# Kernel optimization log

Measured on AMD Instinct MI355X. Metric: run time of the kernel, lower is better.

## Reference

```python
import jax, jax.numpy as jnp
import numpy as np

EMB = 512
HEAD = 64
B, S = 4, 4096


def setup_inputs() -> dict:
    key = jax.random.key(0)
    kq, kk, kv, kwq, kwk, kwv = jax.random.split(key, 6)
    q = jax.random.normal(kq, (B, S, EMB), dtype=jnp.float32)
    k = jax.random.normal(kk, (B, S, EMB), dtype=jnp.float32)
    v = jax.random.normal(kv, (B, S, EMB), dtype=jnp.float32)
    # nn.Linear weights: [out_features, in_features], no bias
    sc = 1.0 / np.sqrt(EMB)
    Wq = jax.random.uniform(kwq, (HEAD, EMB), jnp.float32, -sc, sc)
    Wk = jax.random.uniform(kwk, (HEAD, EMB), jnp.float32, -sc, sc)
    Wv = jax.random.uniform(kwv, (HEAD, EMB), jnp.float32, -sc, sc)
    return {"q": q, "k": k, "v": v, "Wq": Wq, "Wk": Wk, "Wv": Wv}


def reference(q, k, v, Wq, Wk, Wv):
    scale = 1.0 / np.sqrt(HEAD).astype(np.float32)
    Q = jnp.einsum('bse,he->bsh', q, Wq)  # [B,S,HEAD]
    K = jnp.einsum('bse,he->bsh', k, Wk)
    V = jnp.einsum('bse,he->bsh', v, Wv)
    scores = jnp.einsum('bqh,bkh->bqk', Q, K) * scale  # [B,S,S]
    attn = jax.nn.softmax(scores, axis=-1)
    # dropout p=0.0 -> identity
    out = jnp.einsum('bqk,bkh->bqh', attn, V)  # [B,S,HEAD]
    return out
```

## Files before the change

### kernel.cpp

```cpp
#include <hip/hip_runtime.h>
#include <hip/hip_bf16.h>

#define EMB    512
#define HEAD   64
#define SEQ    4096
#define NB     4
#define NSPLIT 8
#define LDX    72

#define SL2E   0.18033688011112042f

typedef __bf16 bf16x8 __attribute__((ext_vector_type(8)));
typedef float  f32x4  __attribute__((ext_vector_type(4)));

__device__ inline ushort4 cvt4(float4 v) {
    __hip_bfloat16 a = __float2bfloat16(v.x), b = __float2bfloat16(v.y);
    __hip_bfloat16 c = __float2bfloat16(v.z), d = __float2bfloat16(v.w);
    ushort4 r;
    r.x = *(unsigned short*)&a; r.y = *(unsigned short*)&b;
    r.z = *(unsigned short*)&c; r.w = *(unsigned short*)&d;
    return r;
}

__global__ __launch_bounds__(256) void cvtw_kernel(
    const float* __restrict__ Wq, const float* __restrict__ Wk,
    const float* __restrict__ Wv, __hip_bfloat16* __restrict__ Wc)
{
    int idx   = blockIdx.x * 256 + threadIdx.x;
    int which = idx >> 13;
    int off   = (idx & 8191) * 4;
    const float* src = (which == 0) ? Wq : (which == 1) ? Wk : Wv;
    float s = (which == 0) ? SL2E : 1.0f;
    float4 v = *(const float4*)(src + off);
    v.x *= s; v.y *= s; v.z *= s; v.w *= s;
    *(ushort4*)(Wc + which * 64 * EMB + off) = cvt4(v);
}

__global__ __launch_bounds__(256) void proj_kernel(
    const float* __restrict__ q, const float* __restrict__ k, const float* __restrict__ v,
    const __hip_bfloat16* __restrict__ Wc,
    __hip_bfloat16* __restrict__ Qo, __hip_bfloat16* __restrict__ Ko,
    __hip_bfloat16* __restrict__ Vto)
{
    __shared__ __hip_bfloat16 Xs[32][LDX];

    const int which = blockIdx.y;
    const float* __restrict__ x = (which == 0) ? q : (which == 1) ? k : v;
    const __hip_bfloat16* __restrict__ W = Wc + which * 64 * EMB;

    const int tid  = threadIdx.x;
    const int wave = tid >> 6, lane = tid & 63;
    const int l16  = lane & 15, quad = lane >> 4;
    const int rs   = (wave & 1) * 16;
    const int ch   = wave >> 1;
    const int r0   = blockIdx.x * 32;
    const float* __restrict__ xb = x + (size_t)r0 * EMB;

    const int sr = tid >> 4;
    const int sc = (tid & 15) << 2;

    const f32x4 z = {0.f, 0.f, 0.f, 0.f};
    f32x4 acc[2] = {z, z};

    float4 xr[2];
    bf16x8 wf[4];

#define LOADX(dst, e0)                                                        \
    _Pragma("unroll")                                                         \
    for (int it = 0; it < 2; ++it)                                            \
        dst[it] = *(const float4*)(xb + (size_t)(it * 16 + sr) * EMB + (e0) + sc);

#define LOADW(dst, e0)                                                        \
    _Pragma("unroll")                                                         \
    for (int st = 0; st < 2; ++st)                                            \
        _Pragma("unroll")                                                     \
        for (int tt = 0; tt < 2; ++tt)                                        \
            dst[st * 2 + tt] = *(const bf16x8*)(W + (size_t)((ch * 2 + tt) * 16 + l16) * EMB \
                                                + (e0) + st * 32 + quad * 8);

    LOADX(xr, 0);
    LOADW(wf, 0);

    #pragma unroll
    for (int c = 0; c < 8; ++c) {
        const int e0 = c * 64;
        if (c) __syncthreads();
        #pragma unroll
        for (int it = 0; it < 2; ++it)
            *(ushort4*)&Xs[it * 16 + sr][sc] = cvt4(xr[it]);
        __syncthreads();

        bf16x8 a0 = *(const bf16x8*)&Xs[rs + l16][quad * 8];
        bf16x8 a1 = *(const bf16x8*)&Xs[rs + l16][32 + quad * 8];

        float4 xr2[2];
        bf16x8 wf2[4];
        if (c < 7) { LOADX(xr2, e0 + 64); LOADW(wf2, e0 + 64); }

        #pragma unroll
        for (int tt = 0; tt < 2; ++tt)
            acc[tt] = __builtin_amdgcn_mfma_f32_16x16x32_bf16(a0, wf[tt], acc[tt], 0, 0, 0);
        #pragma unroll
        for (int tt = 0; tt < 2; ++tt)
            acc[tt] = __builtin_amdgcn_mfma_f32_16x16x32_bf16(a1, wf[2 + tt], acc[tt], 0, 0, 0);

        if (c < 7) {
            #pragma unroll
            for (int it = 0; it < 2; ++it) xr[it] = xr2[it];
            #pragma unroll
            for (int j = 0; j < 4; ++j) wf[j] = wf2[j];
        }
    }
#undef LOADX
#undef LOADW

    #pragma unroll
    for (int tt = 0; tt < 2; ++tt) {
        #pragma unroll
        for (int r = 0; r < 4; ++r) {
            int row = r0 + rs + quad * 4 + r;
            int h   = (ch * 2 + tt) * 16 + l16;
            __hip_bfloat16 val = __float2bfloat16(acc[tt][r]);
            if (which == 0) {
                Qo[(size_t)row * HEAD + h] = val;
            } else if (which == 1) {
                Ko[(size_t)row * HEAD + h] = val;
            } else {
                int b = row >> 12, s = row & (SEQ - 1);
                Vto[((size_t)b * HEAD + h) * SEQ + s] = val;
            }
        }
    }
}

__global__ __launch_bounds__(256, 4) void attn_kernel(
    const __hip_bfloat16* __restrict__ Qb, const __hip_bfloat16* __restrict__ Kb,
    const __hip_bfloat16* __restrict__ Vt, float* __restrict__ Op,
    float* __restrict__ lp)
{
    __shared__ __hip_bfloat16 Ks[64][LDX];
    __shared__ __hip_bfloat16 Vs[64][LDX];
    __shared__ __hip_bfloat16 Ps[128][LDX];

    const int tid  = threadIdx.x;
    const int wave = tid >> 6, lane = tid & 63;
    const int l16  = lane & 15, quad = lane >> 4;
    const int b    = blockIdx.y;
    const int q0   = blockIdx.x * 128;
    const int j0b  = blockIdx.z * (SEQ / NSPLIT);

    bf16x8 qf[2][2];
    #pragma unroll
    for (int s = 0; s < 2; ++s) {
        const __hip_bfloat16* qrow =
            Qb + ((size_t)b * SEQ + q0 + wave * 32 + s * 16 + l16) * HEAD + quad * 8;
        qf[s][0] = *(const bf16x8*)(qrow);
        qf[s][1] = *(const bf16x8*)(qrow + 32);
    }

    const f32x4 z = {0.f, 0.f, 0.f, 0.f};
    f32x4 oacc[2][4] = {{z, z, z, z}, {z, z, z, z}};
    f32x4 lacc[2] = {z, z};

    const __hip_bfloat16 one_bf = __float2bfloat16(1.0f);
    bf16x8 ones;
    #pragma unroll
    for (int j = 0; j < 8; ++j) ones[j] = *(const __bf16*)&one_bf;

    for (int jt = 0; jt < SEQ / NSPLIT; jt += 64) {
        const int j0 = j0b + jt;
        __syncthreads();
        for (int i = tid; i < 512; i += 256) {
            int r = i >> 3, c8 = (i & 7) * 8;
            *(uint4*)&Ks[r][c8] =
                *(const uint4*)(Kb + ((size_t)b * SEQ + j0 + r) * HEAD + c8);
            *(uint4*)&Vs[r][c8] =
                *(const uint4*)(Vt + ((size_t)b * HEAD + r) * SEQ + j0 + c8);
        }
        __syncthreads();

        f32x4 sacc[2][4] = {{z, z, z, z}, {z, z, z, z}};
        #pragma unroll
        for (int st = 0; st < 2; ++st) {
            #pragma unroll
            for (int t = 0; t < 4; ++t) {
                bf16x8 kf = *(const bf16x8*)&Ks[t * 16 + l16][st * 32 + quad * 8];
                #pragma unroll
                for (int s = 0; s < 2; ++s)
                    sacc[s][t] = __builtin_amdgcn_mfma_f32_16x16x32_bf16(kf, qf[s][st], sacc[s][t], 0, 0, 0);
            }
        }

        #pragma unroll
        for (int s = 0; s < 2; ++s)
            #pragma unroll
            for (int t = 0; t < 4; ++t) {
                float4 p;
                p.x = __builtin_amdgcn_exp2f(sacc[s][t][0]);
                p.y = __builtin_amdgcn_exp2f(sacc[s][t][1]);
                p.z = __builtin_amdgcn_exp2f(sacc[s][t][2]);
                p.w = __builtin_amdgcn_exp2f(sacc[s][t][3]);
                *(ushort4*)&Ps[wave * 32 + s * 16 + l16][t * 16 + quad * 4] = cvt4(p);
            }

        #pragma unroll
        for (int s = 0; s < 2; ++s) {
            #pragma unroll
            for (int st = 0; st < 2; ++st) {
                bf16x8 pf = *(const bf16x8*)&Ps[wave * 32 + s * 16 + l16][st * 32 + quad * 8];
                lacc[s] = __builtin_amdgcn_mfma_f32_16x16x32_bf16(pf, ones, lacc[s], 0, 0, 0);
                #pragma unroll
                for (int t = 0; t < 4; ++t) {
                    bf16x8 vf = *(const bf16x8*)&Vs[t * 16 + l16][st * 32 + quad * 8];
                    oacc[s][t] = __builtin_amdgcn_mfma_f32_16x16x32_bf16(pf, vf, oacc[s][t], 0, 0, 0);
                }
            }
        }
    }

    const size_t pb = (size_t)(blockIdx.z * NB + b) * SEQ;
    #pragma unroll
    for (int s = 0; s < 2; ++s) {
        const size_t row0 = pb + q0 + wave * 32 + s * 16 + quad * 4;
        if (l16 == 0) {
            #pragma unroll
            for (int r = 0; r < 4; ++r)
                lp[row0 + r] = lacc[s][r];
        }
        #pragma unroll
        for (int t = 0; t < 4; ++t)
            #pragma unroll
            for (int r = 0; r < 4; ++r)
                Op[(row0 + r) * HEAD + t * 16 + l16] = oacc[s][t][r];
    }
}

__global__ __launch_bounds__(256) void merge_kernel(
    const float* __restrict__ Op, const float* __restrict__ lp,
    float* __restrict__ out)
{
    int idx = blockIdx.x * 256 + threadIdx.x;
    int bq  = idx >> 4;
    int c4  = (idx & 15) * 4;
    float4 acc = {0.f, 0.f, 0.f, 0.f};
    float  l   = 0.f;
    #pragma unroll
    for (int s = 0; s < NSPLIT; ++s) {
        float4 o = *(const float4*)(Op + ((size_t)s * NB * SEQ + bq) * HEAD + c4);
        acc.x += o.x; acc.y += o.y; acc.z += o.z; acc.w += o.w;
        l += lp[(size_t)s * NB * SEQ + bq];
    }
    float inv = 1.f / l;
    float4 r = {acc.x * inv, acc.y * inv, acc.z * inv, acc.w * inv};
    *(float4*)(out + (size_t)bq * HEAD + c4) = r;
}

extern "C" void kernel_launch(void* const* d_in, const int* in_sizes, int n_in,
                              void* d_out, int out_size, void* d_ws, size_t ws_size,
                              hipStream_t stream) {
    const float* q  = (const float*)d_in[0];
    const float* k  = (const float*)d_in[1];
    const float* v  = (const float*)d_in[2];
    const float* Wq = (const float*)d_in[3];
    const float* Wk = (const float*)d_in[4];
    const float* Wv = (const float*)d_in[5];
    float* out = (float*)d_out;

    __hip_bfloat16* Qb = (__hip_bfloat16*)d_ws;
    __hip_bfloat16* Kb = Qb + (size_t)NB * SEQ * HEAD;
    __hip_bfloat16* Vt = Kb + (size_t)NB * SEQ * HEAD;
    __hip_bfloat16* Wc = Vt + (size_t)NB * SEQ * HEAD;
    float* Op = (float*)(Wc + 3 * 64 * EMB);
    float* lp = Op + (size_t)NSPLIT * NB * SEQ * HEAD;

    cvtw_kernel<<<96, 256, 0, stream>>>(Wq, Wk, Wv, Wc);

    dim3 pgrid(NB * SEQ / 32, 3);
    proj_kernel<<<pgrid, dim3(256), 0, stream>>>(q, k, v, Wc, Qb, Kb, Vt);

    dim3 agrid(SEQ / 128, NB, NSPLIT);
    attn_kernel<<<agrid, dim3(256), 0, stream>>>(Qb, Kb, Vt, Op, lp);

    merge_kernel<<<(NB * SEQ * 16) / 256, dim3(256), 0, stream>>>(Op, lp, out);
}
```

Baseline: 172.4 us.

## Double-buffer K/V tiles via direct global-to-LDS loads with XOR swizzle

Replaces the synchronous register-staged K/V tile copies with global_load_lds async loads into double-buffered shared memory, prefetching the next tile while the current one is computed. Shared memory drops the padding in favour of an XOR-swizzled layout to avoid bank conflicts, and the P scratch buffer is shrunk to one 16-row slab per wave that is reused for each sub-tile. The risks are correctness of the manual waitcnt/barrier placement and the reuse of PsF across s iterations without a barrier, which is safe only because each wave touches only its own rows.

```diff
diff --git a/kernel.cpp b/kernel.cpp
--- a/kernel.cpp
+++ b/kernel.cpp
@@ -138,9 +138,9 @@
     const __hip_bfloat16* __restrict__ Vt, float* __restrict__ Op,
     float* __restrict__ lp)
 {
-    __shared__ __hip_bfloat16 Ks[64][LDX];
-    __shared__ __hip_bfloat16 Vs[64][LDX];
-    __shared__ __hip_bfloat16 Ps[128][LDX];
+    __shared__ __hip_bfloat16 KsF[2][64][64];
+    __shared__ __hip_bfloat16 VsF[2][64][64];
+    __shared__ __hip_bfloat16 PsF[64][64];
 
     const int tid  = threadIdx.x;
     const int wave = tid >> 6, lane = tid & 63;
@@ -158,6 +158,30 @@
         qf[s][1] = *(const bf16x8*)(qrow + 32);
     }
 
+    const int rl  = lane >> 3;
+    const int ch8 = (lane & 7) ^ rl;
+    const __hip_bfloat16* __restrict__ Ksrc0 =
+        Kb + ((size_t)b * SEQ + wave * 16 + rl) * HEAD + ch8 * 8;
+    const __hip_bfloat16* __restrict__ Vsrc0 =
+        Vt + ((size_t)b * HEAD + wave * 16 + rl) * SEQ + ch8 * 8;
+
+#define STAGE(bufi, j0)                                                       \
+    do {                                                                      \
+        _Pragma("unroll")                                                     \
+        for (int it = 0; it < 2; ++it) {                                      \
+            __builtin_amdgcn_global_load_lds(                                 \
+                (const __attribute__((address_space(1))) unsigned int*)       \
+                    (const void*)(Ksrc0 + ((size_t)(j0) + it * 8) * HEAD),    \
+                (__attribute__((address_space(3))) unsigned int*)             \
+                    (void*)&KsF[bufi][wave * 16 + it * 8][0], 16, 0, 0);      \
+            __builtin_amdgcn_global_load_lds(                                 \
+                (const __attribute__((address_space(1))) unsigned int*)       \
+                    (const void*)(Vsrc0 + (j0) + (size_t)it * 8 * SEQ),       \
+                (__attribute__((address_space(3))) unsigned int*)             \
+                    (void*)&VsF[bufi][wave * 16 + it * 8][0], 16, 0, 0);      \
+        }                                                                     \
+    } while (0)
+
     const f32x4 z = {0.f, 0.f, 0.f, 0.f};
     f32x4 oacc[2][4] = {{z, z, z, z}, {z, z, z, z}};
     f32x4 lacc[2] = {z, z};
@@ -167,56 +191,71 @@
     #pragma unroll
     for (int j = 0; j < 8; ++j) ones[j] = *(const __bf16*)&one_bf;
 
-    for (int jt = 0; jt < SEQ / NSPLIT; jt += 64) {
-        const int j0 = j0b + jt;
-        __syncthreads();
-        for (int i = tid; i < 512; i += 256) {
-            int r = i >> 3, c8 = (i & 7) * 8;
-            *(uint4*)&Ks[r][c8] =
-                *(const uint4*)(Kb + ((size_t)b * SEQ + j0 + r) * HEAD + c8);
-            *(uint4*)&Vs[r][c8] =
-                *(const uint4*)(Vt + ((size_t)b * HEAD + r) * SEQ + j0 + c8);
-        }
-        __syncthreads();
-
-        f32x4 sacc[2][4] = {{z, z, z, z}, {z, z, z, z}};
-        #pragma unroll
-        for (int st = 0; st < 2; ++st) {
-            #pragma unroll
-            for (int t = 0; t < 4; ++t) {
-                bf16x8 kf = *(const bf16x8*)&Ks[t * 16 + l16][st * 32 + quad * 8];
+    STAGE(0, j0b);
+
+    const int xs = l16 & 7;
+
+    #pragma unroll
+    for (int jt = 0; jt < SEQ / NSPLIT / 64; ++jt) {
+        const int cur = jt & 1;
+        if (jt < SEQ / NSPLIT / 64 - 1) {
+            STAGE(cur ^ 1, j0b + (jt + 1) * 64);
+            asm volatile("s_waitcnt vmcnt(4)" ::: "memory");
+        } else {
+            asm volatile("s_waitcnt vmcnt(0)" ::: "memory");
+        }
+        __builtin_amdgcn_sched_barrier(0);
+        __builtin_amdgcn_s_barrier();
+        asm volatile("" ::: "memory");
+
+        #pragma unroll
+        for (int s = 0; s < 2; ++s) {
+            f32x4 sacc[4] = {z, z, z, z};
+            #pragma unroll
+            for (int st = 0; st < 2; ++st)
                 #pragma unroll
-                for (int s = 0; s < 2; ++s)
-                    sacc[s][t] = __builtin_amdgcn_mfma_f32_16x16x32_bf16(kf, qf[s][st], sacc[s][t], 0, 0, 0);
-            }
-        }
-
-        #pragma unroll
-        for (int s = 0; s < 2; ++s)
+                for (int t = 0; t < 4; ++t) {
+                    bf16x8 kf = *(const bf16x8*)
+                        &KsF[cur][t * 16 + l16][((st * 4 + quad) ^ xs) * 8];
+                    sacc[t] = __builtin_amdgcn_mfma_f32_16x16x32_bf16(kf, qf[s][st], sacc[t], 0, 0, 0);
+                }
+
+            asm volatile("" ::: "memory");
+            __builtin_amdgcn_sched_barrier(0);
+
             #pragma unroll
             for (int t = 0; t < 4; ++t) {
                 float4 p;
-                p.x = __builtin_amdgcn_exp2f(sacc[s][t][0]);
-                p.y = __builtin_amdgcn_exp2f(sacc[s][t][1]);
-                p.z = __builtin_amdgcn_exp2f(sacc[s][t][2]);
-                p.w = __builtin_amdgcn_exp2f(sacc[s][t][3]);
-                *(ushort4*)&Ps[wave * 32 + s * 16 + l16][t * 16 + quad * 4] = cvt4(p);
+                p.x = __builtin_amdgcn_exp2f(sacc[t][0]);
+                p.y = __builtin_amdgcn_exp2f(sacc[t][1]);
+                p.z = __builtin_amdgcn_exp2f(sacc[t][2]);
+                p.w = __builtin_amdgcn_exp2f(sacc[t][3]);
+                *(ushort4*)&PsF[wave * 16 + l16]
+                    [(((t * 2 + (quad >> 1)) ^ xs) * 8) + (quad & 1) * 4] = cvt4(p);
             }
 
-        #pragma unroll
-        for (int s = 0; s < 2; ++s) {
+            asm volatile("" ::: "memory");
+            __builtin_amdgcn_sched_barrier(0);
+
             #pragma unroll
             for (int st = 0; st < 2; ++st) {
-                bf16x8 pf = *(const bf16x8*)&Ps[wave * 32 + s * 16 + l16][st * 32 + quad * 8];
+                bf16x8 pf = *(const bf16x8*)
+                    &PsF[wave * 16 + l16][((st * 4 + quad) ^ xs) * 8];
                 lacc[s] = __builtin_amdgcn_mfma_f32_16x16x32_bf16(pf, ones, lacc[s], 0, 0, 0);
                 #pragma unroll
                 for (int t = 0; t < 4; ++t) {
-                    bf16x8 vf = *(const bf16x8*)&Vs[t * 16 + l16][st * 32 + quad * 8];
+                    bf16x8 vf = *(const bf16x8*)
+                        &VsF[cur][t * 16 + l16][((st * 4 + quad) ^ xs) * 8];
                     oacc[s][t] = __builtin_amdgcn_mfma_f32_16x16x32_bf16(pf, vf, oacc[s][t], 0, 0, 0);
                 }
             }
         }
-    }
+        asm volatile("s_waitcnt lgkmcnt(0)" ::: "memory");
+        __builtin_amdgcn_sched_barrier(0);
+        __builtin_amdgcn_s_barrier();
+        asm volatile("" ::: "memory");
+    }
+#undef STAGE
 
     const size_t pb = (size_t)(blockIdx.z * NB + b) * SEQ;
     #pragma unroll
```

Measured after the change: 171.6 us. No clear change (-0.4%).
